# Optimization experiments

Measured on AMD Instinct MI355X. Metric: run time of the kernel, lower is better.

The kernel has to match this reference:

```python
import jax, jax.numpy as jnp
import numpy as np

B, L, D, NH = 4, 1024, 1024, 16
DH = D // NH
H = 8 * D // 3  # SwiGLU hidden = 2730
NEG = -1e9


def setup_inputs() -> dict:
    key = jax.random.key(0)
    ks = jax.random.split(key, 8)
    init = lambda k, shape: (jax.random.normal(k, shape, jnp.float32) * 0.02)
    x = jax.random.normal(ks[0], (B, L, D), jnp.float32)
    causal = jnp.tril(jnp.ones((L, L), bool))
    m = jnp.where(causal, 0.0, NEG)[None, None].astype(jnp.float32)  # [1,1,L,L]
    return {
        'x': x,
        'm': m,
        'wx': init(ks[1], (D, 3 * D)),
        'bx': jnp.zeros((3 * D,), jnp.float32),
        'wo': init(ks[2], (D, D)),
        'bo': jnp.zeros((D,), jnp.float32),
        'mhanorm_w': jnp.ones((D,), jnp.float32),
        'ffnorm_w': jnp.ones((D,), jnp.float32),
        'u': init(ks[3], (D, H)),
        'v': init(ks[4], (D, H)),
        'w': init(ks[5], (H, D)),
    }


def rmsnorm(x, weight, eps=1e-8):
    rrms = jax.lax.rsqrt(jnp.mean(x * x, axis=-1, keepdims=True) + eps)
    return weight * x * rrms


def reference(x, m, wx, bx, wo, bo, mhanorm_w, ffnorm_w, u, v, w):
    scale = D ** (-0.5)  # note: original uses d**-0.5, NOT dh**-0.5
    qkv = rmsnorm(x, mhanorm_w) @ wx + bx                 # [B,L,3D]
    q, k, vv = jnp.split(qkv, 3, axis=-1)                  # each [B,L,D]
    split = lambda t: t.reshape(B, L, NH, DH).transpose(0, 2, 1, 3)  # [B,NH,L,DH]
    q, k, vv = split(q), split(k), split(vv)               # pe = identity (default)
    scores = jnp.einsum('bhic,bhjc->bhij', q, k) * scale + m
    A = jax.nn.softmax(scores, axis=-1)
    head = jnp.einsum('bhij,bhjc->bhic', A, vv)            # [B,NH,L,DH]
    head = head.transpose(0, 2, 1, 3).reshape(B, L, D)
    x = x + head @ wo + bo
    xn = rmsnorm(x, ffnorm_w)
    return x + (jax.nn.silu(xn @ u) * (xn @ v)) @ w
```

## Files before the change

### kernel.cpp

```cpp
#include <hip/hip_runtime.h>

#define B_  4
#define L_  1024
#define D_  1024
#define NH_ 16
#define DH_ 64
#define H_  2730
#define HP_ 2816
#define M_  4096

typedef short bf16x8 __attribute__((ext_vector_type(8)));
typedef float f32x4  __attribute__((ext_vector_type(4)));

__device__ __forceinline__ unsigned short f2bf(float f) {
    unsigned int u = __builtin_bit_cast(unsigned int, f);
    u += 0x7fffu + ((u >> 16) & 1u);
    return (unsigned short)(u >> 16);
}
__device__ __forceinline__ float bf2f(unsigned short s) {
    unsigned int u = ((unsigned int)s) << 16;
    return __builtin_bit_cast(float, u);
}

__device__ __forceinline__ void glds16(const void* g, void* l) {
    __builtin_amdgcn_global_load_lds(
        (const __attribute__((address_space(1))) unsigned int*)g,
        (__attribute__((address_space(3))) unsigned int*)l, 16, 0, 0);
}

__global__ __launch_bounds__(256) void cvtT_kernel(
    const float* __restrict__ in, unsigned short* __restrict__ out,
    int K, int N, int Kp, int Np)
{
    __shared__ float t[32][33];
    const int k0 = blockIdx.x * 32, n0 = blockIdx.y * 32;
    const int tx = threadIdx.x & 31, ty = threadIdx.x >> 5;
    #pragma unroll
    for (int i = 0; i < 4; ++i) {
        const int k = k0 + ty + i * 8, n = n0 + tx;
        t[ty + i * 8][tx] = (k < K && n < N) ? in[(size_t)k * N + n] : 0.0f;
    }
    __syncthreads();
    #pragma unroll
    for (int i = 0; i < 4; ++i) {
        const int n = n0 + ty + i * 8, k = k0 + tx;
        out[(size_t)n * Kp + k] = f2bf(t[tx][ty + i * 8]);
    }
}

__global__ __launch_bounds__(256) void rmsnorm_kernel(
    const float* __restrict__ x, const float* __restrict__ w,
    unsigned short* __restrict__ out)
{
    const int row = blockIdx.x;
    const int t = threadIdx.x;
    const float4 v = ((const float4*)(x + (size_t)row * 1024))[t];
    float ss = v.x*v.x + v.y*v.y + v.z*v.z + v.w*v.w;
    #pragma unroll
    for (int off = 32; off > 0; off >>= 1) ss += __shfl_down(ss, off);
    __shared__ float red[4];
    if ((t & 63) == 0) red[t >> 6] = ss;
    __syncthreads();
    const float tot = red[0] + red[1] + red[2] + red[3];
    const float rr = rsqrtf(tot * (1.0f / 1024.0f) + 1e-8f);
    const float4 wv = ((const float4*)w)[t];
    ushort4 o;
    o.x = f2bf(v.x * wv.x * rr); o.y = f2bf(v.y * wv.y * rr);
    o.z = f2bf(v.z * wv.z * rr); o.w = f2bf(v.w * wv.w * rr);
    ((ushort4*)(out + (size_t)row * 1024))[t] = o;
}

template<int EPI, int TN>
__global__ __launch_bounds__(256) void gemm_bf16(
    const unsigned short* __restrict__ A, const unsigned short* __restrict__ Bt,
    int M, int N, int K,
    const float* __restrict__ bias, const float* __restrict__ res,
    const unsigned short* __restrict__ mul,
    float* __restrict__ outf, unsigned short* __restrict__ outb)
{
    constexpr int NS = TN / 32;
    constexpr int G  = (TN == 128) ? 4 : 3;
    constexpr int WAIT_G = 0xF70 | G;
    __shared__ __align__(16) unsigned short As[2][128 * 32];
    __shared__ __align__(16) unsigned short Bs[2][TN * 32];
    const int tid = threadIdx.x;
    const int m0 = blockIdx.y * 128, n0 = blockIdx.x * TN;
    const int lane = tid & 63, w = tid >> 6;
    const int wm = w >> 1, wn = w & 1;
    const int quad = lane >> 4, l15 = lane & 15;

    f32x4 acc[4][NS] = {};

    const int p0 = w * 64 + lane;
    const int r0 = p0 >> 2, c0 = (p0 & 3) ^ (r0 & 3);
    const int offL0 = p0 * 8, offL1 = 2048 + p0 * 8;

    const unsigned short* Ag0 = A + (size_t)(m0 + r0) * K + c0 * 8;
    const unsigned short* Ag1 = A + (size_t)(m0 + 64 + r0) * K + c0 * 8;
    const unsigned short* Bg0 = Bt + (size_t)(n0 + r0) * K + c0 * 8;
    const unsigned short* Bg1 = Bt + (size_t)(n0 + 64 + r0) * K + c0 * 8;

    auto stage = [&](int kk, int buf) {
        glds16(Ag0 + kk, &As[buf][offL0]);
        glds16(Ag1 + kk, &As[buf][offL1]);
        glds16(Bg0 + kk, &Bs[buf][offL0]);
        if (TN == 128) glds16(Bg1 + kk, &Bs[buf][offL1]);
    };
    auto compute = [&](int buf) {
        bf16x8 af[4], bfr[NS];
        #pragma unroll
        for (int ms = 0; ms < 4; ++ms) {
            const int row = wm * 64 + ms * 16 + l15;
            af[ms] = *(const bf16x8*)&As[buf][row * 32 + ((quad ^ (row & 3)) * 8)];
        }
        #pragma unroll
        for (int ns = 0; ns < NS; ++ns) {
            const int row = wn * (TN / 2) + ns * 16 + l15;
            bfr[ns] = *(const bf16x8*)&Bs[buf][row * 32 + ((quad ^ (row & 3)) * 8)];
        }
        #pragma unroll
        for (int ms = 0; ms < 4; ++ms)
            #pragma unroll
            for (int ns = 0; ns < NS; ++ns)
                acc[ms][ns] = __builtin_amdgcn_mfma_f32_16x16x32_bf16(
                    af[ms], bfr[ns], acc[ms][ns], 0, 0, 0);
    };

    const int nk = K >> 5;
    stage(0, 0);
    for (int i = 0; i < nk; i += 2) {
        if (i + 1 < nk) { stage((i + 1) << 5, 1); __builtin_amdgcn_s_waitcnt(WAIT_G); }
        else            { __builtin_amdgcn_s_waitcnt(0xF70); }
        __builtin_amdgcn_s_barrier();
        compute(0);
        __builtin_amdgcn_s_barrier();
        if (i + 2 < nk) { stage((i + 2) << 5, 0); __builtin_amdgcn_s_waitcnt(WAIT_G); }
        else            { __builtin_amdgcn_s_waitcnt(0xF70); }
        __builtin_amdgcn_s_barrier();
        compute(1);
        __builtin_amdgcn_s_barrier();
    }

    #pragma unroll
    for (int ms = 0; ms < 4; ++ms) {
        #pragma unroll
        for (int r = 0; r < 4; ++r) {
            const int row = m0 + wm * 64 + ms * 16 + quad * 4 + r;
            const size_t ro = (size_t)row * N;
            #pragma unroll
            for (int ns = 0; ns < NS; ++ns) {
                const int col = n0 + wn * (TN / 2) + ns * 16 + l15;
                float v = acc[ms][ns][r];
                if (EPI == 0) {
                    outb[ro + col] = f2bf(v + bias[col]);
                } else if (EPI == 1) {
                    outf[ro + col] = v + bias[col] + res[ro + col];
                } else if (EPI == 2) {
                    outb[ro + col] = f2bf(v);
                } else if (EPI == 3) {
                    float t = bf2f(mul[ro + col]);
                    float g = v / (1.0f + __expf(-v)) * t;
                    outb[ro + col] = f2bf(g);
                } else {
                    outf[ro + col] = v + res[ro + col];
                }
            }
        }
    }
}

__global__ __launch_bounds__(256) void attn_mfma_kernel(
    const unsigned short* __restrict__ qkv, unsigned short* __restrict__ hout)
{
    __shared__ __align__(16) unsigned short Qs[128 * 72];
    __shared__ __align__(16) unsigned short Ks[64 * 72];
    __shared__ __align__(16) unsigned short Vt[64 * 72];
    __shared__ __align__(16) unsigned short Ps[128 * 72];

    const int tid = threadIdx.x;
    const int qt = blockIdx.x, h = blockIdx.y, b = blockIdx.z;
    const int q0 = qt * 128;
    const int w = tid >> 6, lane = tid & 63;
    const int quad = lane >> 4, l15 = lane & 15;

    {
        const int row = tid >> 1, half = tid & 1;
        const unsigned short* gp = qkv + (size_t)(b * L_ + q0 + row) * 3072 + h * 64 + half * 32;
        uint4 a = *(const uint4*)gp;
        uint4 c = *(const uint4*)(gp + 8);
        uint4 d = *(const uint4*)(gp + 16);
        uint4 e = *(const uint4*)(gp + 24);
        unsigned short* dp = &Qs[row * 72 + half * 32];
        *(uint4*)dp = a; *(uint4*)(dp + 8) = c; *(uint4*)(dp + 16) = d; *(uint4*)(dp + 24) = e;
    }

    f32x4 O[2][4] = {};
    float m_st[2][4], l_st[2][4];
    #pragma unroll
    for (int qs = 0; qs < 2; ++qs)
        #pragma unroll
        for (int r = 0; r < 4; ++r) { m_st[qs][r] = -1e30f; l_st[qs][r] = 0.0f; }

    const int ktiles = 2 * qt + 2;
    const int wave_qmax = q0 + w * 32 + 31;
    const int krow = tid >> 2, kseg = tid & 3;
    const int vkey = (tid & 31) * 2, vdp = tid >> 5;

    for (int kt = 0; kt < ktiles; ++kt) {
        const int k0 = kt * 64;
        __syncthreads();
        {
            const unsigned short* gp = qkv + (size_t)(b * L_ + k0 + krow) * 3072 + 1024 + h * 64 + kseg * 16;
            uint4 a = *(const uint4*)gp;
            uint4 c = *(const uint4*)(gp + 8);
            unsigned short* dp = &Ks[krow * 72 + kseg * 16];
            *(uint4*)dp = a; *(uint4*)(dp + 8) = c;
        }
        {
            const unsigned short* gp = qkv + (size_t)(b * L_ + k0 + vkey) * 3072 + 2048 + h * 64 + vdp * 8;
            union { uint4 u; unsigned short s[8]; } v0, v1;
            v0.u = *(const uint4*)gp;
            v1.u = *(const uint4*)(gp + 3072);
            #pragma unroll
            for (int i = 0; i < 8; ++i) {
                unsigned int pk = (unsigned int)v0.s[i] | ((unsigned int)v1.s[i] << 16);
                *(unsigned int*)&Vt[(vdp * 8 + i) * 72 + vkey] = pk;
            }
        }
        __syncthreads();

        if (k0 <= wave_qmax) {
            bf16x8 af[2][2], bfk[4][2];
            #pragma unroll
            for (int qs = 0; qs < 2; ++qs)
                #pragma unroll
                for (int s = 0; s < 2; ++s)
                    af[qs][s] = *(const bf16x8*)&Qs[(w * 32 + qs * 16 + l15) * 72 + s * 32 + quad * 8];
            #pragma unroll
            for (int n = 0; n < 4; ++n)
                #pragma unroll
                for (int s = 0; s < 2; ++s)
                    bfk[n][s] = *(const bf16x8*)&Ks[(n * 16 + l15) * 72 + s * 32 + quad * 8];
            f32x4 sacc[2][4] = {};
            #pragma unroll
            for (int qs = 0; qs < 2; ++qs)
                #pragma unroll
                for (int n = 0; n < 4; ++n) {
                    sacc[qs][n] = __builtin_amdgcn_mfma_f32_16x16x32_bf16(af[qs][0], bfk[n][0], sacc[qs][n], 0, 0, 0);
                    sacc[qs][n] = __builtin_amdgcn_mfma_f32_16x16x32_bf16(af[qs][1], bfk[n][1], sacc[qs][n], 0, 0, 0);
                }

            #pragma unroll
            for (int qs = 0; qs < 2; ++qs) {
                const int rowg0 = q0 + w * 32 + qs * 16 + quad * 4;
                float p[4][4], mx[4];
                #pragma unroll
                for (int r = 0; r < 4; ++r) mx[r] = -1e30f;
                #pragma unroll
                for (int n = 0; n < 4; ++n) {
                    const int col = k0 + n * 16 + l15;
                    #pragma unroll
                    for (int r = 0; r < 4; ++r) {
                        float v = sacc[qs][n][r] * 0.03125f;
                        if (col > rowg0 + r) v = -1e30f;
                        p[n][r] = v;
                        mx[r] = fmaxf(mx[r], v);
                    }
                }
                #pragma unroll
                for (int r = 0; r < 4; ++r) {
                    #pragma unroll
                    for (int m = 1; m < 16; m <<= 1)
                        mx[r] = fmaxf(mx[r], __shfl_xor(mx[r], m));
                }
                float alpha[4], rs[4];
                #pragma unroll
                for (int r = 0; r < 4; ++r) {
                    const float mnew = fmaxf(m_st[qs][r], mx[r]);
                    alpha[r] = __expf(m_st[qs][r] - mnew);
                    m_st[qs][r] = mnew;
                    float s0 = 0.0f;
                    #pragma unroll
                    for (int n = 0; n < 4; ++n) {
                        const float e = __expf(p[n][r] - mnew);
                        p[n][r] = e;
                        s0 += e;
                    }
                    rs[r] = s0;
                }
                #pragma unroll
                for (int r = 0; r < 4; ++r) {
                    #pragma unroll
                    for (int m = 1; m < 16; m <<= 1)
                        rs[r] += __shfl_xor(rs[r], m);
                    l_st[qs][r] = l_st[qs][r] * alpha[r] + rs[r];
                }
                #pragma unroll
                for (int dn = 0; dn < 4; ++dn)
                    #pragma unroll
                    for (int r = 0; r < 4; ++r)
                        O[qs][dn][r] *= alpha[r];
                #pragma unroll
                for (int n = 0; n < 4; ++n)
                    #pragma unroll
                    for (int r = 0; r < 4; ++r)
                        Ps[(w * 32 + qs * 16 + quad * 4 + r) * 72 + n * 16 + l15] = f2bf(p[n][r]);
            }

            bf16x8 ap[2][2], bv[4][2];
            #pragma unroll
            for (int qs = 0; qs < 2; ++qs)
                #pragma unroll
                for (int s = 0; s < 2; ++s)
                    ap[qs][s] = *(const bf16x8*)&Ps[(w * 32 + qs * 16 + l15) * 72 + s * 32 + quad * 8];
            #pragma unroll
            for (int dn = 0; dn < 4; ++dn)
                #pragma unroll
                for (int s = 0; s < 2; ++s)
                    bv[dn][s] = *(const bf16x8*)&Vt[(dn * 16 + l15) * 72 + s * 32 + quad * 8];
            #pragma unroll
            for (int qs = 0; qs < 2; ++qs)
                #pragma unroll
                for (int dn = 0; dn < 4; ++dn) {
                    O[qs][dn] = __builtin_amdgcn_mfma_f32_16x16x32_bf16(ap[qs][0], bv[dn][0], O[qs][dn], 0, 0, 0);
                    O[qs][dn] = __builtin_amdgcn_mfma_f32_16x16x32_bf16(ap[qs][1], bv[dn][1], O[qs][dn], 0, 0, 0);
                }
        }
    }

    #pragma unroll
    for (int qs = 0; qs < 2; ++qs) {
        #pragma unroll
        for (int r = 0; r < 4; ++r) {
            const float inv = 1.0f / l_st[qs][r];
            const int rowg = q0 + w * 32 + qs * 16 + quad * 4 + r;
            unsigned short* op = hout + (size_t)(b * L_ + rowg) * 1024 + h * 64;
            #pragma unroll
            for (int dn = 0; dn < 4; ++dn)
                op[dn * 16 + l15] = f2bf(O[qs][dn][r] * inv);
        }
    }
}

extern "C" void kernel_launch(void* const* d_in, const int* in_sizes, int n_in,
                              void* d_out, int out_size, void* d_ws, size_t ws_size,
                              hipStream_t stream)
{
    const float* x   = (const float*)d_in[0];
    const float* wx  = (const float*)d_in[2];
    const float* bx  = (const float*)d_in[3];
    const float* wo  = (const float*)d_in[4];
    const float* bo  = (const float*)d_in[5];
    const float* mhw = (const float*)d_in[6];
    const float* ffw = (const float*)d_in[7];
    const float* u   = (const float*)d_in[8];
    const float* v   = (const float*)d_in[9];
    const float* w   = (const float*)d_in[10];
    float* out = (float*)d_out;

    char* W = (char*)d_ws;
    unsigned short* xn_bf   = (unsigned short*)(W + 0);
    unsigned short* wx_bf   = (unsigned short*)(W + 8388608);
    unsigned short* qkv_bf  = (unsigned short*)(W + 14680064);
    unsigned short* head_bf = (unsigned short*)(W + 39845888);
    unsigned short* wo_bf   = (unsigned short*)(W + 48234496);
    float*          x2      = (float*)(W + 50331648);
    unsigned short* u_bf    = (unsigned short*)(W + 67108864);
    unsigned short* v_bf    = (unsigned short*)(W + 72876032);
    unsigned short* w_bf    = (unsigned short*)(W + 78643200);
    unsigned short* g_bf    = (unsigned short*)(W + 84410368);
    unsigned short* tv_bf   = qkv_bf;

    cvtT_kernel<<<dim3(32, 96), 256, 0, stream>>>(wx, wx_bf, 1024, 3072, 1024, 3072);
    cvtT_kernel<<<dim3(32, 32), 256, 0, stream>>>(wo, wo_bf, 1024, 1024, 1024, 1024);
    cvtT_kernel<<<dim3(32, 88), 256, 0, stream>>>(u,  u_bf, 1024, 2730, 1024, 2816);
    cvtT_kernel<<<dim3(32, 88), 256, 0, stream>>>(v,  v_bf, 1024, 2730, 1024, 2816);
    cvtT_kernel<<<dim3(88, 32), 256, 0, stream>>>(w,  w_bf, 2730, 1024, 2816, 1024);

    rmsnorm_kernel<<<4096, 256, 0, stream>>>(x, mhw, xn_bf);

    gemm_bf16<0, 128><<<dim3(3072 / 128, 32), 256, 0, stream>>>(
        xn_bf, wx_bf, 4096, 3072, 1024, bx, nullptr, nullptr, nullptr, qkv_bf);

    attn_mfma_kernel<<<dim3(8, 16, 4), 256, 0, stream>>>(qkv_bf, head_bf);

    gemm_bf16<1, 64><<<dim3(1024 / 64, 32), 256, 0, stream>>>(
        head_bf, wo_bf, 4096, 1024, 1024, bo, x, nullptr, x2, nullptr);

    rmsnorm_kernel<<<4096, 256, 0, stream>>>(x2, ffw, xn_bf);

    gemm_bf16<2, 128><<<dim3(2816 / 128, 32), 256, 0, stream>>>(
        xn_bf, v_bf, 4096, 2816, 1024, nullptr, nullptr, nullptr, nullptr, tv_bf);

    gemm_bf16<3, 128><<<dim3(2816 / 128, 32), 256, 0, stream>>>(
        xn_bf, u_bf, 4096, 2816, 1024, nullptr, nullptr, tv_bf, nullptr, g_bf);

    gemm_bf16<4, 64><<<dim3(1024 / 64, 32), 256, 0, stream>>>(
        g_bf, w_bf, 4096, 1024, 2816, nullptr, x2, nullptr, out, nullptr);
}
```

Baseline: 386.3 us.

## Pair causal query tiles per block and double-buffer K/V in attention

Each attention block now handles two 64-row query tiles (qa and 15-qa), so every block does the same 17 key-tile iterations and the causal workload is balanced. K is staged asynchronously into a swizzled double buffer via glds16, and V is prefetched into registers and written to the second buffer. This overlaps the next tile's loads with the current compute and needs one barrier per iteration instead of two. Each wave now owns 16 query rows instead of 32, which lowers the MFMA work per K/V load and adds bookkeeping to switch query tiles mid-loop.

```diff
diff --git a/kernel.cpp b/kernel.cpp
--- a/kernel.cpp
+++ b/kernel.cpp
@@ -169,176 +169,211 @@
     }
 }
 
-__global__ __launch_bounds__(256) void attn_mfma_kernel(
+__global__ __launch_bounds__(256) void attn_mfma2_kernel(
     const unsigned short* __restrict__ qkv, unsigned short* __restrict__ hout)
 {
-    __shared__ __align__(16) unsigned short Qs[128 * 72];
-    __shared__ __align__(16) unsigned short Ks[64 * 72];
-    __shared__ __align__(16) unsigned short Vt[64 * 72];
-    __shared__ __align__(16) unsigned short Ps[128 * 72];
+    __shared__ __align__(16) unsigned short Qs[2][64 * 72];
+    __shared__ __align__(16) unsigned short Ks[2][64 * 64];
+    __shared__ __align__(16) unsigned short Vt[2][64 * 72];
+    __shared__ __align__(16) unsigned short Ps[64 * 68];
 
     const int tid = threadIdx.x;
-    const int qt = blockIdx.x, h = blockIdx.y, b = blockIdx.z;
-    const int q0 = qt * 128;
+    const int qa = blockIdx.x, h = blockIdx.y, b = blockIdx.z;
+    const int qb = 15 - qa;
     const int w = tid >> 6, lane = tid & 63;
     const int quad = lane >> 4, l15 = lane & 15;
 
+    const size_t basek = (size_t)(b * L_) * 3072 + 1024 + h * 64;
+    const size_t basev = basek + 1024;
+
     {
         const int row = tid >> 1, half = tid & 1;
-        const unsigned short* gp = qkv + (size_t)(b * L_ + q0 + row) * 3072 + h * 64 + half * 32;
+        const int tile = row >> 6, r6 = row & 63;
+        const int grow = (tile ? qb : qa) * 64 + r6;
+        const unsigned short* gp = qkv + (size_t)(b * L_ + grow) * 3072 + h * 64 + half * 32;
         uint4 a = *(const uint4*)gp;
         uint4 c = *(const uint4*)(gp + 8);
         uint4 d = *(const uint4*)(gp + 16);
         uint4 e = *(const uint4*)(gp + 24);
-        unsigned short* dp = &Qs[row * 72 + half * 32];
+        unsigned short* dp = &Qs[tile][r6 * 72 + half * 32];
         *(uint4*)dp = a; *(uint4*)(dp + 8) = c; *(uint4*)(dp + 16) = d; *(uint4*)(dp + 24) = e;
     }
 
-    f32x4 O[2][4] = {};
-    float m_st[2][4], l_st[2][4];
-    #pragma unroll
-    for (int qs = 0; qs < 2; ++qs)
-        #pragma unroll
-        for (int r = 0; r < 4; ++r) { m_st[qs][r] = -1e30f; l_st[qs][r] = 0.0f; }
-
-    const int ktiles = 2 * qt + 2;
-    const int wave_qmax = q0 + w * 32 + 31;
-    const int krow = tid >> 2, kseg = tid & 3;
+    auto stageK = [&](int kt, int buf) {
+        #pragma unroll
+        for (int i = 0; i < 2; ++i) {
+            const int p = i * 256 + tid;
+            const int row = p >> 3;
+            const int cc = (p & 7) ^ (row & 7);
+            glds16(qkv + basek + (size_t)(kt * 64 + row) * 3072 + cc * 8, &Ks[buf][p * 8]);
+        }
+    };
     const int vkey = (tid & 31) * 2, vdp = tid >> 5;
-
-    for (int kt = 0; kt < ktiles; ++kt) {
-        const int k0 = kt * 64;
-        __syncthreads();
-        {
-            const unsigned short* gp = qkv + (size_t)(b * L_ + k0 + krow) * 3072 + 1024 + h * 64 + kseg * 16;
-            uint4 a = *(const uint4*)gp;
-            uint4 c = *(const uint4*)(gp + 8);
-            unsigned short* dp = &Ks[krow * 72 + kseg * 16];
-            *(uint4*)dp = a; *(uint4*)(dp + 8) = c;
-        }
-        {
-            const unsigned short* gp = qkv + (size_t)(b * L_ + k0 + vkey) * 3072 + 2048 + h * 64 + vdp * 8;
-            union { uint4 u; unsigned short s[8]; } v0, v1;
-            v0.u = *(const uint4*)gp;
-            v1.u = *(const uint4*)(gp + 3072);
-            #pragma unroll
-            for (int i = 0; i < 8; ++i) {
-                unsigned int pk = (unsigned int)v0.s[i] | ((unsigned int)v1.s[i] << 16);
-                *(unsigned int*)&Vt[(vdp * 8 + i) * 72 + vkey] = pk;
+    auto loadV = [&](int kt, uint4& v0, uint4& v1) {
+        const unsigned short* gp = qkv + basev + (size_t)(kt * 64 + vkey) * 3072 + vdp * 8;
+        v0 = *(const uint4*)gp;
+        v1 = *(const uint4*)(gp + 3072);
+    };
+    auto writeV = [&](int buf, const uint4& v0, const uint4& v1) {
+        union { uint4 u; unsigned short s[8]; } a, c;
+        a.u = v0; c.u = v1;
+        #pragma unroll
+        for (int i = 0; i < 8; ++i) {
+            unsigned int pk = (unsigned int)a.s[i] | ((unsigned int)c.s[i] << 16);
+            *(unsigned int*)&Vt[buf][(vdp * 8 + i) * 72 + vkey] = pk;
+        }
+    };
+
+    f32x4 O[4] = {};
+    float m4[4], l4[4];
+    #pragma unroll
+    for (int r = 0; r < 4; ++r) { m4[r] = -1e30f; l4[r] = 0.0f; }
+
+    stageK(0, 0);
+    {
+        uint4 v0, v1;
+        loadV(0, v0, v1);
+        writeV(0, v0, v1);
+    }
+    __syncthreads();
+
+    bf16x8 af[2];
+    #pragma unroll
+    for (int s = 0; s < 2; ++s)
+        af[s] = *(const bf16x8*)&Qs[0][(w * 16 + l15) * 72 + s * 32 + quad * 8];
+
+    int qsel = 0, kt = 0;
+    for (int t = 0; t < 17; ++t) {
+        const int cb = t & 1, nb = cb ^ 1;
+        const bool havenext = (t < 16);
+        uint4 nv0, nv1;
+        if (havenext) {
+            const int ktn = (t + 1 <= qa) ? (t + 1) : (t - qa);
+            stageK(ktn, nb);
+            loadV(ktn, nv0, nv1);
+        }
+
+        bf16x8 bfk[4][2];
+        #pragma unroll
+        for (int n = 0; n < 4; ++n) {
+            const int row = n * 16 + l15;
+            #pragma unroll
+            for (int s = 0; s < 2; ++s)
+                bfk[n][s] = *(const bf16x8*)&Ks[cb][row * 64 + (((s * 4 + quad) ^ (row & 7)) * 8)];
+        }
+        f32x4 sacc[4] = {};
+        #pragma unroll
+        for (int n = 0; n < 4; ++n) {
+            sacc[n] = __builtin_amdgcn_mfma_f32_16x16x32_bf16(af[0], bfk[n][0], sacc[n], 0, 0, 0);
+            sacc[n] = __builtin_amdgcn_mfma_f32_16x16x32_bf16(af[1], bfk[n][1], sacc[n], 0, 0, 0);
+        }
+
+        const bool diag = (kt == (qsel ? qb : qa));
+        float p[4][4], mx[4];
+        #pragma unroll
+        for (int r = 0; r < 4; ++r) mx[r] = -1e30f;
+        #pragma unroll
+        for (int n = 0; n < 4; ++n) {
+            const int col = n * 16 + l15;
+            #pragma unroll
+            for (int r = 0; r < 4; ++r) {
+                float v = sacc[n][r] * 0.03125f;
+                if (diag && col > (w * 16 + quad * 4 + r)) v = -1e30f;
+                p[n][r] = v;
+                mx[r] = fmaxf(mx[r], v);
             }
         }
-        __syncthreads();
-
-        if (k0 <= wave_qmax) {
-            bf16x8 af[2][2], bfk[4][2];
-            #pragma unroll
-            for (int qs = 0; qs < 2; ++qs)
-                #pragma unroll
-                for (int s = 0; s < 2; ++s)
-                    af[qs][s] = *(const bf16x8*)&Qs[(w * 32 + qs * 16 + l15) * 72 + s * 32 + quad * 8];
-            #pragma unroll
-            for (int n = 0; n < 4; ++n)
-                #pragma unroll
-                for (int s = 0; s < 2; ++s)
-                    bfk[n][s] = *(const bf16x8*)&Ks[(n * 16 + l15) * 72 + s * 32 + quad * 8];
-            f32x4 sacc[2][4] = {};
-            #pragma unroll
-            for (int qs = 0; qs < 2; ++qs)
-                #pragma unroll
-                for (int n = 0; n < 4; ++n) {
-                    sacc[qs][n] = __builtin_amdgcn_mfma_f32_16x16x32_bf16(af[qs][0], bfk[n][0], sacc[qs][n], 0, 0, 0);
-                    sacc[qs][n] = __builtin_amdgcn_mfma_f32_16x16x32_bf16(af[qs][1], bfk[n][1], sacc[qs][n], 0, 0, 0);
-                }
-
-            #pragma unroll
-            for (int qs = 0; qs < 2; ++qs) {
-                const int rowg0 = q0 + w * 32 + qs * 16 + quad * 4;
-                float p[4][4], mx[4];
-                #pragma unroll
-                for (int r = 0; r < 4; ++r) mx[r] = -1e30f;
-                #pragma unroll
-                for (int n = 0; n < 4; ++n) {
-                    const int col = k0 + n * 16 + l15;
-                    #pragma unroll
-                    for (int r = 0; r < 4; ++r) {
-                        float v = sacc[qs][n][r] * 0.03125f;
-                        if (col > rowg0 + r) v = -1e30f;
-                        p[n][r] = v;
-                        mx[r] = fmaxf(mx[r], v);
-                    }
-                }
-                #pragma unroll
-                for (int r = 0; r < 4; ++r) {
-                    #pragma unroll
-                    for (int m = 1; m < 16; m <<= 1)
-                        mx[r] = fmaxf(mx[r], __shfl_xor(mx[r], m));
-                }
-                float alpha[4], rs[4];
-                #pragma unroll
-                for (int r = 0; r < 4; ++r) {
-                    const float mnew = fmaxf(m_st[qs][r], mx[r]);
-                    alpha[r] = __expf(m_st[qs][r] - mnew);
-                    m_st[qs][r] = mnew;
-                    float s0 = 0.0f;
-                    #pragma unroll
-                    for (int n = 0; n < 4; ++n) {
-                        const float e = __expf(p[n][r] - mnew);
-                        p[n][r] = e;
-                        s0 += e;
-                    }
-                    rs[r] = s0;
-                }
-                #pragma unroll
-                for (int r = 0; r < 4; ++r) {
-                    #pragma unroll
-                    for (int m = 1; m < 16; m <<= 1)
-                        rs[r] += __shfl_xor(rs[r], m);
-                    l_st[qs][r] = l_st[qs][r] * alpha[r] + rs[r];
-                }
+        #pragma unroll
+        for (int r = 0; r < 4; ++r) {
+            #pragma unroll
+            for (int m = 1; m < 16; m <<= 1)
+                mx[r] = fmaxf(mx[r], __shfl_xor(mx[r], m));
+        }
+        float alpha[4], rs[4];
+        #pragma unroll
+        for (int r = 0; r < 4; ++r) {
+            const float mnew = fmaxf(m4[r], mx[r]);
+            alpha[r] = __expf(m4[r] - mnew);
+            m4[r] = mnew;
+            float s0 = 0.0f;
+            #pragma unroll
+            for (int n = 0; n < 4; ++n) {
+                const float e = __expf(p[n][r] - mnew);
+                p[n][r] = e;
+                s0 += e;
+            }
+            rs[r] = s0;
+        }
+        #pragma unroll
+        for (int r = 0; r < 4; ++r) {
+            #pragma unroll
+            for (int m = 1; m < 16; m <<= 1)
+                rs[r] += __shfl_xor(rs[r], m);
+            l4[r] = l4[r] * alpha[r] + rs[r];
+        }
+        #pragma unroll
+        for (int dn = 0; dn < 4; ++dn)
+            #pragma unroll
+            for (int r = 0; r < 4; ++r)
+                O[dn][r] *= alpha[r];
+        #pragma unroll
+        for (int n = 0; n < 4; ++n)
+            #pragma unroll
+            for (int r = 0; r < 4; ++r)
+                Ps[(w * 16 + quad * 4 + r) * 68 + n * 16 + l15] = f2bf(p[n][r]);
+
+        if (havenext) writeV(nb, nv0, nv1);
+
+        bf16x8 ap[2], bv[4][2];
+        #pragma unroll
+        for (int s = 0; s < 2; ++s)
+            ap[s] = *(const bf16x8*)&Ps[(w * 16 + l15) * 68 + s * 32 + quad * 8];
+        #pragma unroll
+        for (int dn = 0; dn < 4; ++dn)
+            #pragma unroll
+            for (int s = 0; s < 2; ++s)
+                bv[dn][s] = *(const bf16x8*)&Vt[cb][(dn * 16 + l15) * 72 + s * 32 + quad * 8];
+        #pragma unroll
+        for (int dn = 0; dn < 4; ++dn) {
+            O[dn] = __builtin_amdgcn_mfma_f32_16x16x32_bf16(ap[0], bv[dn][0], O[dn], 0, 0, 0);
+            O[dn] = __builtin_amdgcn_mfma_f32_16x16x32_bf16(ap[1], bv[dn][1], O[dn], 0, 0, 0);
+        }
+
+        if (t == qa) {
+            #pragma unroll
+            for (int r = 0; r < 4; ++r) {
+                const float inv = 1.0f / l4[r];
+                const int grow = qa * 64 + w * 16 + quad * 4 + r;
+                unsigned short* op = hout + (size_t)(b * L_ + grow) * 1024 + h * 64;
                 #pragma unroll
                 for (int dn = 0; dn < 4; ++dn)
-                    #pragma unroll
-                    for (int r = 0; r < 4; ++r)
-                        O[qs][dn][r] *= alpha[r];
-                #pragma unroll
-                for (int n = 0; n < 4; ++n)
-                    #pragma unroll
-                    for (int r = 0; r < 4; ++r)
-                        Ps[(w * 32 + qs * 16 + quad * 4 + r) * 72 + n * 16 + l15] = f2bf(p[n][r]);
+                    op[dn * 16 + l15] = f2bf(O[dn][r] * inv);
             }
-
-            bf16x8 ap[2][2], bv[4][2];
-            #pragma unroll
-            for (int qs = 0; qs < 2; ++qs)
-                #pragma unroll
-                for (int s = 0; s < 2; ++s)
-                    ap[qs][s] = *(const bf16x8*)&Ps[(w * 32 + qs * 16 + l15) * 72 + s * 32 + quad * 8];
             #pragma unroll
             for (int dn = 0; dn < 4; ++dn)
                 #pragma unroll
-                for (int s = 0; s < 2; ++s)
-                    bv[dn][s] = *(const bf16x8*)&Vt[(dn * 16 + l15) * 72 + s * 32 + quad * 8];
-            #pragma unroll
-            for (int qs = 0; qs < 2; ++qs)
-                #pragma unroll
-                for (int dn = 0; dn < 4; ++dn) {
-                    O[qs][dn] = __builtin_amdgcn_mfma_f32_16x16x32_bf16(ap[qs][0], bv[dn][0], O[qs][dn], 0, 0, 0);
-                    O[qs][dn] = __builtin_amdgcn_mfma_f32_16x16x32_bf16(ap[qs][1], bv[dn][1], O[qs][dn], 0, 0, 0);
-                }
-        }
-    }
-
-    #pragma unroll
-    for (int qs = 0; qs < 2; ++qs) {
-        #pragma unroll
-        for (int r = 0; r < 4; ++r) {
-            const float inv = 1.0f / l_st[qs][r];
-            const int rowg = q0 + w * 32 + qs * 16 + quad * 4 + r;
-            unsigned short* op = hout + (size_t)(b * L_ + rowg) * 1024 + h * 64;
-            #pragma unroll
-            for (int dn = 0; dn < 4; ++dn)
-                op[dn * 16 + l15] = f2bf(O[qs][dn][r] * inv);
-        }
+                for (int r = 0; r < 4; ++r) O[dn][r] = 0.0f;
+            #pragma unroll
+            for (int r = 0; r < 4; ++r) { m4[r] = -1e30f; l4[r] = 0.0f; }
+            qsel = 1;
+            kt = 0;
+            #pragma unroll
+            for (int s = 0; s < 2; ++s)
+                af[s] = *(const bf16x8*)&Qs[1][(w * 16 + l15) * 72 + s * 32 + quad * 8];
+        } else {
+            ++kt;
+        }
+        __syncthreads();
+    }
+
+    #pragma unroll
+    for (int r = 0; r < 4; ++r) {
+        const float inv = 1.0f / l4[r];
+        const int grow = qb * 64 + w * 16 + quad * 4 + r;
+        unsigned short* op = hout + (size_t)(b * L_ + grow) * 1024 + h * 64;
+        #pragma unroll
+        for (int dn = 0; dn < 4; ++dn)
+            op[dn * 16 + l15] = f2bf(O[dn][r] * inv);
     }
 }
 
@@ -382,7 +417,7 @@
     gemm_bf16<0, 128><<<dim3(3072 / 128, 32), 256, 0, stream>>>(
         xn_bf, wx_bf, 4096, 3072, 1024, bx, nullptr, nullptr, nullptr, qkv_bf);
 
-    attn_mfma_kernel<<<dim3(8, 16, 4), 256, 0, stream>>>(qkv_bf, head_bf);
+    attn_mfma2_kernel<<<dim3(8, 16, 4), 256, 0, stream>>>(qkv_bf, head_bf);
 
     gemm_bf16<1, 64><<<dim3(1024 / 64, 32), 256, 0, stream>>>(
         head_bf, wo_bf, 4096, 1024, 1024, bo, x, nullptr, x2, nullptr);
```

After: 364.1 us. -5.7%, faster.
